# Performance work log

Measured on AMD Instinct MI355X. Metric: run time of the kernel, lower is better.

## Reference

```python
import jax, jax.numpy as jnp
import numpy as np

N = 20000      # nodes
E = 256000     # edges
H = 8          # heads
DIN = 256      # in_dim_struct / in_dim_semantic
DH = 32        # num_hidden per head (H*DH == DIN for GT residual)
PRED = 32      # pred_dim (relation embedding dim)
REL = 16       # rel_num
NEG = 0.2      # negative_slope for GAT attention
ALPHA = 0.5    # args.fusion
NUM_LAYERS = 2


def seg_softmax(e, seg, n):
    # softmax over edges grouped by destination node; e: [E, ...], seg: [E]
    m = jax.ops.segment_max(e, seg, num_segments=n)
    ex = jnp.exp(e - m[seg])
    s = jax.ops.segment_sum(ex, seg, num_segments=n)
    return ex / (s[seg] + 1e-9)


def setup_inputs() -> dict:
    key = jax.random.key(0)
    ks = jax.random.split(key, 24)
    f32 = jnp.float32
    def rn(k, shape, scale=0.05):
        return jax.random.normal(k, shape, dtype=f32) * scale
    return {
        "feats_struct": jax.random.normal(ks[0], (N, DIN), f32),
        "feats_semantic": jax.random.normal(ks[1], (N, DIN), f32),
        "centrality": jax.random.uniform(ks[2], (N,), f32),
        # fused per-head scoring MLP (heads[0] small Sequentials batched over H)
        "Ws1": rn(ks[3], (H, DIN, DIN // 2)),
        "bs1": jnp.zeros((H, DIN // 2), f32),
        "Ws2": rn(ks[4], (H, DIN // 2)),
        "bs2": jnp.zeros((H,), f32),
        "rel_emb": rn(ks[5], (REL, PRED), 1.0),
        # SALayer params (2 layers, per-head scalar channels)
        "sa_w": rn(ks[6], (NUM_LAYERS, H), 1.0),
        "sa_al": rn(ks[7], (NUM_LAYERS, H), 1.0),
        "sa_ar": rn(ks[8], (NUM_LAYERS, H), 1.0),
        "sa_We": rn(ks[9], (NUM_LAYERS, PRED, H)),
        # GTLayer params
        "Wq": rn(ks[10], (DIN, H * DH)),
        "bq": jnp.zeros((H * DH,), f32),
        "Wk": rn(ks[11], (DIN, H * DH)),
        "bk": jnp.zeros((H * DH,), f32),
        "Wv": rn(ks[12], (DIN, H * DH)),
        "bv": jnp.zeros((H * DH,), f32),
        "We_gt": rn(ks[13], (PRED, H * DH)),
        "bn_gamma": jnp.ones((H * DH,), f32),
        "bn_beta": jnp.zeros((H * DH,), f32),
        "Wout": rn(ks[14], (H * DH, 1)),
        "bout": jnp.zeros((1,), f32),
        # centrality scale params
        "gamma": jnp.ones((1, H), f32),
        "beta": jnp.zeros((1, H), f32),
        "edge_types": jax.random.randint(ks[15], (E,), 0, REL),
        "edge_src": jax.random.randint(ks[16], (E,), 0, N),
        "edge_dst": jax.random.randint(ks[17], (E,), 0, N),
    }


def _forward(feats_struct, feats_semantic, centrality, Ws1, bs1, Ws2, bs2,
             rel_emb, sa_w, sa_al, sa_ar, sa_We, Wq, bq, Wk, bk, Wv, bv,
             We_gt, bn_gamma, bn_beta, Wout, bout, gamma, beta,
             edge_types, edge_src, edge_dst):
    n = feats_struct.shape[0]
    edge_feats = rel_emb[edge_types]                                   # [E, PRED]

    # ---- structural channel: fused per-head scoring MLPs ----
    h1 = jax.nn.relu(jnp.einsum('nd,hdk->nhk', feats_struct, Ws1) + bs1)  # [N,H,DIN/2]
    h = jnp.einsum('nhk,hk->nh', h1, Ws2) + bs2                           # [N,H]

    # ---- SALayer stack (GAT-style, per-head scalar features) ----
    for l in range(NUM_LAYERS):
        z = h * sa_w[l]                                                 # [N,H]
        e = jax.nn.leaky_relu(z[edge_src] * sa_al[l] + z[edge_dst] * sa_ar[l]
                              + edge_feats @ sa_We[l], NEG)             # [E,H]
        attn = seg_softmax(e, edge_dst, n)                              # [E,H]
        out = jax.ops.segment_sum(attn * z[edge_src], edge_dst, num_segments=n)
        h = jax.nn.elu(out + z)                                         # residual + activation
        if l != NUM_LAYERS - 1:
            h = jnp.mean(h, axis=-1, keepdims=True)
            h = jnp.tile(h, (1, H))
    logits_struct = h                                                   # [N,H]

    # ---- semantic channel: Graph Transformer layer (edge_mode='MUL') ----
    q = (feats_semantic @ Wq + bq).reshape(n, H, DH)
    k = (feats_semantic @ Wk + bk).reshape(n, H, DH)
    v = (feats_semantic @ Wv + bv).reshape(n, H, DH)
    ep = (edge_feats @ We_gt).reshape(-1, H, DH)                        # [E,H,DH]
    ke = k[edge_src] * ep                                               # MUL edge gating
    score = jnp.sum(q[edge_dst] * ke, axis=-1) / jnp.sqrt(jnp.float32(DH))  # [E,H]
    attn = seg_softmax(score, edge_dst, n)                              # [E,H]
    agg = jax.ops.segment_sum(attn[..., None] * v[edge_src], edge_dst,
                              num_segments=n).reshape(n, H * DH)
    agg = agg + feats_semantic                                          # residual (H*DH == DIN)
    mu = jnp.mean(agg, axis=0)
    var = jnp.var(agg, axis=0)
    agg = (agg - mu) / jnp.sqrt(var + 1e-5) * bn_gamma + bn_beta        # batch norm
    h_sem = jax.nn.relu(agg)
    logits_semantic = h_sem @ Wout + bout                               # [N,1]

    # ---- fusion + centrality gamma/beta scaling ----
    logits = ALPHA * logits_struct + (1.0 - ALPHA) * logits_semantic    # [N,H]
    scaled = (centrality[:, None] * gamma + beta) * logits              # [N,H]
    return jax.nn.leaky_relu(jnp.mean(scaled, axis=-1, keepdims=True), 0.01)


def reference(feats_struct, feats_semantic, centrality, Ws1, bs1, Ws2, bs2,
              rel_emb, sa_w, sa_al, sa_ar, sa_We, Wq, bq, Wk, bk, Wv, bv,
              We_gt, bn_gamma, bn_beta, Wout, bout, gamma, beta,
              edge_types, edge_src, edge_dst):
    return _forward(feats_struct, feats_semantic, centrality, Ws1, bs1, Ws2, bs2,
                    rel_emb, sa_w, sa_al, sa_ar, sa_We, Wq, bq, Wk, bk, Wv, bv,
                    We_gt, bn_gamma, bn_beta, Wout, bout, gamma, beta,
                    edge_types, edge_src, edge_dst)
```

## Files before the change

kernel.cpp:

```cpp
#include <hip/hip_runtime.h>
#include <hip/hip_bf16.h>
#include <math.h>

#define N_NODES 20000
#define N_EDGES 256000

typedef __attribute__((ext_vector_type(8))) __bf16 bf16x8;
typedef __attribute__((ext_vector_type(8))) unsigned short u16x8;
typedef __attribute__((ext_vector_type(4))) float f32x4;

static __device__ __forceinline__ unsigned short f2bf(float f) {
  unsigned u = __float_as_uint(f);
  unsigned r = (u + 0x7fffu + ((u >> 16) & 1u)) >> 16;
  return (unsigned short)r;
}


__global__ void k_tables(const float* __restrict__ rel_emb,
                         const float* __restrict__ sa_We,
                         const float* __restrict__ We_gt,
                         float* __restrict__ saTab, float* __restrict__ epTab) {
  int t = threadIdx.x;
  {
    int l = t >> 7, r = (t >> 3) & 15, h = t & 7;
    float acc = 0.f;
    for (int p = 0; p < 32; ++p)
      acc += rel_emb[r * 32 + p] * sa_We[l * 256 + p * 8 + h];
    saTab[t] = acc;
  }
  for (int r = 0; r < 16; ++r) {
    float acc = 0.f;
    for (int p = 0; p < 32; ++p)
      acc += rel_emb[r * 32 + p] * We_gt[p * 256 + t];
    epTab[r * 256 + t] = acc;
  }
}

__global__ void k_hist(const int* __restrict__ e_dst, int* __restrict__ deg) {
  int e = blockIdx.x * 256 + threadIdx.x;
  if (e < N_EDGES) atomicAdd(&deg[e_dst[e]], 1);
}

__global__ void k_scan(const int* __restrict__ deg, int* __restrict__ rowPtr,
                       int* __restrict__ cursor) {
  const int CH = (N_NODES + 255) / 256;
  int t = threadIdx.x;
  int b0 = t * CH, b1 = min(b0 + CH, N_NODES);
  int s = 0;
  for (int i = b0; i < b1; ++i) s += deg[i];
  __shared__ int part[256];
  part[t] = s;
  __syncthreads();
  for (int off = 1; off < 256; off <<= 1) {
    int add = (t >= off) ? part[t - off] : 0;
    __syncthreads();
    part[t] += add;
    __syncthreads();
  }
  int run = (t == 0) ? 0 : part[t - 1];
  for (int i = b0; i < b1; ++i) {
    rowPtr[i] = run;
    cursor[i] = run;
    run += deg[i];
  }
  if (t == 0) rowPtr[N_NODES] = part[255];
}

__global__ void k_fill(const int* __restrict__ e_dst, const int* __restrict__ e_src,
                       const int* __restrict__ e_type, int* __restrict__ cursor,
                       int* __restrict__ csrSrc, int* __restrict__ csrType) {
  int e = blockIdx.x * 256 + threadIdx.x;
  if (e >= N_EDGES) return;
  int d = e_dst[e];
  int pos = atomicAdd(&cursor[d], 1);
  csrSrc[pos] = e_src[e];
  csrType[pos] = e_type[e];
}


__global__ void k_convX(const float* __restrict__ Xs, const float* __restrict__ Xm,
                        ushort* __restrict__ Xsb, ushort* __restrict__ Xmb) {
  size_t i = ((size_t)blockIdx.x * 256 + threadIdx.x) * 4;
  float4 a = *(const float4*)(Xs + i);
  ushort4 ua = {f2bf(a.x), f2bf(a.y), f2bf(a.z), f2bf(a.w)};
  *(ushort4*)(Xsb + i) = ua;
  float4 b = *(const float4*)(Xm + i);
  ushort4 ub = {f2bf(b.x), f2bf(b.y), f2bf(b.z), f2bf(b.w)};
  *(ushort4*)(Xmb + i) = ub;
}

__global__ void k_tws1(const float* __restrict__ Ws1, ushort* __restrict__ Ws1t) {
  int h = blockIdx.x >> 7, kcol = blockIdx.x & 127, d = threadIdx.x;
  Ws1t[((size_t)h * 128 + kcol) * 256 + d] = f2bf(Ws1[((size_t)h * 256 + d) * 128 + kcol]);
}

__global__ void k_twqkv(const float* __restrict__ Wq, const float* __restrict__ Wk,
                        const float* __restrict__ Wv, ushort* __restrict__ Wt) {
  int m = blockIdx.x >> 8, n = blockIdx.x & 255, d = threadIdx.x;
  const float* W = (m == 0) ? Wq : (m == 1) ? Wk : Wv;
  Wt[((size_t)m * 256 + n) * 256 + d] = f2bf(W[(size_t)d * 256 + n]);
}


__global__ __launch_bounds__(256) void k_mlp_mfma(
    const ushort* __restrict__ Xb, const ushort* __restrict__ Ws1t,
    const float* __restrict__ bs1, const float* __restrict__ Ws2,
    const float* __restrict__ bs2, float* __restrict__ h0) {
  __shared__ ushort Ab[64][136];
  __shared__ ushort Bb[128][136];
  int tid = threadIdx.x;
  int h = blockIdx.y;
  int base = blockIdx.x * 64;
  int wv = tid >> 6, lane = tid & 63;
  int l15 = lane & 15, lhi = lane >> 4;
  f32x4 acc[8];
  #pragma unroll
  for (int nt = 0; nt < 8; ++nt) acc[nt] = (f32x4){0.f, 0.f, 0.f, 0.f};

  for (int kc = 0; kc < 2; ++kc) {
    {
      int r = tid >> 2, c4 = (tid & 3) * 4;
      int gr = base + r;
      const ushort* src = Xb + (size_t)gr * 256 + kc * 128;
      #pragma unroll
      for (int s = 0; s < 4; ++s) {
        u16x8 val = {0, 0, 0, 0, 0, 0, 0, 0};
        if (gr < N_NODES) val = *(const u16x8*)(src + (c4 + s) * 8);
        *(u16x8*)&Ab[r][(c4 + s) * 8] = val;
      }
    }
    {
      int r = tid >> 1, cb = (tid & 1) * 8;
      const ushort* src = Ws1t + ((size_t)h * 128 + r) * 256 + kc * 128;
      #pragma unroll
      for (int s = 0; s < 8; ++s)
        *(u16x8*)&Bb[r][(cb + s) * 8] = *(const u16x8*)(src + (cb + s) * 8);
    }
    __syncthreads();
    #pragma unroll
    for (int kk = 0; kk < 4; ++kk) {
      bf16x8 a = *(const bf16x8*)&Ab[wv * 16 + l15][kk * 32 + lhi * 8];
      #pragma unroll
      for (int nt = 0; nt < 8; ++nt) {
        bf16x8 b = *(const bf16x8*)&Bb[nt * 16 + l15][kk * 32 + lhi * 8];
        acc[nt] = __builtin_amdgcn_mfma_f32_16x16x32_bf16(a, b, acc[nt], 0, 0, 0);
      }
    }
    __syncthreads();
  }
  float part[4] = {0.f, 0.f, 0.f, 0.f};
  #pragma unroll
  for (int nt = 0; nt < 8; ++nt) {
    int c = h * 128 + nt * 16 + l15;
    float b1 = bs1[c], w2 = Ws2[c];
    #pragma unroll
    for (int j = 0; j < 4; ++j)
      part[j] += fmaxf(acc[nt][j] + b1, 0.f) * w2;
  }
  #pragma unroll
  for (int j = 0; j < 4; ++j) {
    #pragma unroll
    for (int o = 1; o < 16; o <<= 1) part[j] += __shfl_xor(part[j], o);
  }
  if (l15 == 0) {
    float b2 = bs2[h];
    #pragma unroll
    for (int j = 0; j < 4; ++j) {
      int row = base + wv * 16 + lhi * 4 + j;
      if (row < N_NODES) h0[(size_t)row * 8 + h] = part[j] + b2;
    }
  }
}


__global__ __launch_bounds__(256) void k_qkv_mfma(
    const ushort* __restrict__ Xb, const ushort* __restrict__ Wt,
    const float* __restrict__ bq, const float* __restrict__ bk,
    const float* __restrict__ bv, float* __restrict__ q,
    float* __restrict__ k, float* __restrict__ v) {
  __shared__ ushort Ab[64][136];
  __shared__ ushort Bb[128][136];
  int tid = threadIdx.x;
  int m = blockIdx.y >> 1, half = blockIdx.y & 1;
  int base = blockIdx.x * 64;
  int wv = tid >> 6, lane = tid & 63;
  int l15 = lane & 15, lhi = lane >> 4;
  f32x4 acc[8];
  #pragma unroll
  for (int nt = 0; nt < 8; ++nt) acc[nt] = (f32x4){0.f, 0.f, 0.f, 0.f};

  for (int kc = 0; kc < 2; ++kc) {
    {
      int r = tid >> 2, c4 = (tid & 3) * 4;
      int gr = base + r;
      const ushort* src = Xb + (size_t)gr * 256 + kc * 128;
      #pragma unroll
      for (int s = 0; s < 4; ++s) {
        u16x8 val = {0, 0, 0, 0, 0, 0, 0, 0};
        if (gr < N_NODES) val = *(const u16x8*)(src + (c4 + s) * 8);
        *(u16x8*)&Ab[r][(c4 + s) * 8] = val;
      }
    }
    {
      int r = tid >> 1, cb = (tid & 1) * 8;
      const ushort* src = Wt + (((size_t)m * 256 + half * 128 + r) * 256) + kc * 128;
      #pragma unroll
      for (int s = 0; s < 8; ++s)
        *(u16x8*)&Bb[r][(cb + s) * 8] = *(const u16x8*)(src + (cb + s) * 8);
    }
    __syncthreads();
    #pragma unroll
    for (int kk = 0; kk < 4; ++kk) {
      bf16x8 a = *(const bf16x8*)&Ab[wv * 16 + l15][kk * 32 + lhi * 8];
      #pragma unroll
      for (int nt = 0; nt < 8; ++nt) {
        bf16x8 b = *(const bf16x8*)&Bb[nt * 16 + l15][kk * 32 + lhi * 8];
        acc[nt] = __builtin_amdgcn_mfma_f32_16x16x32_bf16(a, b, acc[nt], 0, 0, 0);
      }
    }
    __syncthreads();
  }
  float* out = (m == 0) ? q : (m == 1) ? k : v;
  const float* bias = (m == 0) ? bq : (m == 1) ? bk : bv;
  #pragma unroll
  for (int nt = 0; nt < 8; ++nt) {
    int c = half * 128 + nt * 16 + l15;
    float bc = bias[c];
    #pragma unroll
    for (int j = 0; j < 4; ++j) {
      int row = base + wv * 16 + lhi * 4 + j;
      if (row < N_NODES) out[(size_t)row * 256 + c] = acc[nt][j] + bc;
    }
  }
}


__global__ __launch_bounds__(256) void k_sa(const float* __restrict__ h_in,
                                            float* __restrict__ h_out,
                                            const int* __restrict__ rowPtr,
                                            const int* __restrict__ csrSrc,
                                            const int* __restrict__ csrType,
                                            const float* __restrict__ sa_w,
                                            const float* __restrict__ sa_al,
                                            const float* __restrict__ sa_ar,
                                            const float* __restrict__ saTab, int layer) {
  int t = blockIdx.x * 256 + threadIdx.x;
  int node = t >> 3, h = t & 7;
  float wgt = sa_w[layer * 8 + h];
  float al = sa_al[layer * 8 + h];
  float ar = sa_ar[layer * 8 + h];
  const float* tab = saTab + layer * 128;
  float zd = h_in[node * 8 + h] * wgt;
  int s0 = rowPtr[node], s1 = rowPtr[node + 1];
  float m = -INFINITY, lsum = 0.f, acc = 0.f;
  for (int i = s0; i < s1; ++i) {
    int s = csrSrc[i], ty = csrType[i];
    float zs = h_in[s * 8 + h] * wgt;
    float e = zs * al + zd * ar + tab[ty * 8 + h];
    e = (e >= 0.f) ? e : 0.2f * e;
    float nm = fmaxf(m, e);
    float scl = expf(m - nm);
    float p = expf(e - nm);
    acc = acc * scl + p * zs;
    lsum = lsum * scl + p;
    m = nm;
  }
  float o = acc / (lsum + 1e-9f);
  float r = o + zd;
  r = (r > 0.f) ? r : expm1f(r);
  if (layer == 0) {
    r += __shfl_xor(r, 1);
    r += __shfl_xor(r, 2);
    r += __shfl_xor(r, 4);
    r *= 0.125f;
  }
  h_out[node * 8 + h] = r;
}


__global__ __launch_bounds__(256) void k_gt(const float* __restrict__ q,
                                            const float* __restrict__ k,
                                            const float* __restrict__ v,
                                            const float* __restrict__ epTab,
                                            const float* __restrict__ feats_sem,
                                            const int* __restrict__ rowPtr,
                                            const int* __restrict__ csrSrc,
                                            const int* __restrict__ csrType,
                                            float* __restrict__ agg) {
  int node = blockIdx.x * 4 + (threadIdx.x >> 6);
  int lane = threadIdx.x & 63;
  int c0 = lane * 4;
  const float SC = 0.17677669529663687f;
  float4 qv = *(const float4*)(q + (size_t)node * 256 + c0);
  qv.x *= SC; qv.y *= SC; qv.z *= SC; qv.w *= SC;
  float4 acc = {0.f, 0.f, 0.f, 0.f};
  float m = -INFINITY, lsum = 0.f;
  int s0 = rowPtr[node], s1 = rowPtr[node + 1];
  for (int i = s0; i < s1; ++i) {
    int s = csrSrc[i], ty = csrType[i];
    float4 kv = *(const float4*)(k + (size_t)s * 256 + c0);
    float4 ep = *(const float4*)(epTab + ty * 256 + c0);
    float part = qv.x * kv.x * ep.x + qv.y * kv.y * ep.y +
                 qv.z * kv.z * ep.z + qv.w * kv.w * ep.w;
    part += __shfl_xor(part, 1);
    part += __shfl_xor(part, 2);
    part += __shfl_xor(part, 4);
    float nm = fmaxf(m, part);
    float scl = expf(m - nm);
    float p = expf(part - nm);
    float4 vv = *(const float4*)(v + (size_t)s * 256 + c0);
    acc.x = acc.x * scl + p * vv.x;
    acc.y = acc.y * scl + p * vv.y;
    acc.z = acc.z * scl + p * vv.z;
    acc.w = acc.w * scl + p * vv.w;
    lsum = lsum * scl + p;
    m = nm;
  }
  float inv = 1.f / (lsum + 1e-9f);
  float4 fs = *(const float4*)(feats_sem + (size_t)node * 256 + c0);
  float4 r;
  r.x = acc.x * inv + fs.x;
  r.y = acc.y * inv + fs.y;
  r.z = acc.z * inv + fs.z;
  r.w = acc.w * inv + fs.w;
  *(float4*)(agg + (size_t)node * 256 + c0) = r;
}

__global__ void k_bnstats(const float* __restrict__ agg, double* __restrict__ colsum,
                          double* __restrict__ colssq) {
  int t = threadIdx.x;
  int r0 = blockIdx.x * 79;
  int r1 = min(r0 + 79, N_NODES);
  double s = 0.0, qq = 0.0;
  for (int r = r0; r < r1; ++r) {
    float x = agg[(size_t)r * 256 + t];
    s += (double)x;
    qq += (double)x * (double)x;
  }
  atomicAdd(&colsum[t], s);
  atomicAdd(&colssq[t], qq);
}

__global__ void k_bnfinal(const double* __restrict__ colsum, const double* __restrict__ colssq,
                          float* __restrict__ muArr, float* __restrict__ invArr) {
  int t = threadIdx.x;
  double mu = colsum[t] / (double)N_NODES;
  double var = colssq[t] / (double)N_NODES - mu * mu;
  muArr[t] = (float)mu;
  invArr[t] = (float)(1.0 / sqrt(var + 1e-5));
}

__global__ __launch_bounds__(256) void k_final(const float* __restrict__ agg,
                                               const float* __restrict__ muArr,
                                               const float* __restrict__ invArr,
                                               const float* __restrict__ bn_gamma,
                                               const float* __restrict__ bn_beta,
                                               const float* __restrict__ Wout,
                                               const float* __restrict__ bout,
                                               const float* __restrict__ hB,
                                               const float* __restrict__ cent,
                                               const float* __restrict__ gamma,
                                               const float* __restrict__ beta,
                                               float* __restrict__ out) {
  int node = blockIdx.x * 4 + (threadIdx.x >> 6);
  int lane = threadIdx.x & 63;
  int c0 = lane * 4;
  float4 x = *(const float4*)(agg + (size_t)node * 256 + c0);
  float4 mu = *(const float4*)(muArr + c0);
  float4 iv = *(const float4*)(invArr + c0);
  float4 g = *(const float4*)(bn_gamma + c0);
  float4 b = *(const float4*)(bn_beta + c0);
  float4 w = *(const float4*)(Wout + c0);
  float p = fmaxf((x.x - mu.x) * iv.x * g.x + b.x, 0.f) * w.x +
            fmaxf((x.y - mu.y) * iv.y * g.y + b.y, 0.f) * w.y +
            fmaxf((x.z - mu.z) * iv.z * g.z + b.z, 0.f) * w.z +
            fmaxf((x.w - mu.w) * iv.w * g.w + b.w, 0.f) * w.w;
  #pragma unroll
  for (int o = 1; o < 64; o <<= 1) p += __shfl_xor(p, o);
  float ls = p + bout[0];
  int h = lane & 7;
  float logit = 0.5f * hB[(size_t)node * 8 + h] + 0.5f * ls;
  float sc = (cent[node] * gamma[h] + beta[h]) * logit;
  sc += __shfl_xor(sc, 1);
  sc += __shfl_xor(sc, 2);
  sc += __shfl_xor(sc, 4);
  float mn = sc * 0.125f;
  mn = (mn >= 0.f) ? mn : 0.01f * mn;
  if (lane == 0) out[node] = mn;
}


extern "C" void kernel_launch(void* const* d_in, const int* in_sizes, int n_in,
                              void* d_out, int out_size, void* d_ws, size_t ws_size,
                              hipStream_t stream) {
  (void)in_sizes; (void)n_in; (void)out_size; (void)ws_size;
  const float* feats_struct = (const float*)d_in[0];
  const float* feats_sem    = (const float*)d_in[1];
  const float* cent         = (const float*)d_in[2];
  const float* Ws1          = (const float*)d_in[3];
  const float* bs1          = (const float*)d_in[4];
  const float* Ws2          = (const float*)d_in[5];
  const float* bs2          = (const float*)d_in[6];
  const float* rel_emb      = (const float*)d_in[7];
  const float* sa_w         = (const float*)d_in[8];
  const float* sa_al        = (const float*)d_in[9];
  const float* sa_ar        = (const float*)d_in[10];
  const float* sa_We        = (const float*)d_in[11];
  const float* Wq           = (const float*)d_in[12];
  const float* bq           = (const float*)d_in[13];
  const float* Wk           = (const float*)d_in[14];
  const float* bk           = (const float*)d_in[15];
  const float* Wv           = (const float*)d_in[16];
  const float* bv           = (const float*)d_in[17];
  const float* We_gt        = (const float*)d_in[18];
  const float* bn_gamma     = (const float*)d_in[19];
  const float* bn_beta      = (const float*)d_in[20];
  const float* Wout         = (const float*)d_in[21];
  const float* bout         = (const float*)d_in[22];
  const float* gamma        = (const float*)d_in[23];
  const float* beta         = (const float*)d_in[24];
  const int* e_type         = (const int*)d_in[25];
  const int* e_src          = (const int*)d_in[26];
  const int* e_dst          = (const int*)d_in[27];
  float* out = (float*)d_out;

  char* wsb = (char*)d_ws;
  size_t off = 0;
  auto alloc = [&](size_t bytes) -> char* {
    char* p = wsb + off;
    off = (off + bytes + 255) & ~(size_t)255;
    return p;
  };
  float* saTab   = (float*)alloc(2 * 16 * 8 * 4);
  float* epTab   = (float*)alloc(16 * 256 * 4);
  int* deg       = (int*)alloc((size_t)N_NODES * 4);
  int* rowPtr    = (int*)alloc((size_t)(N_NODES + 1) * 4);
  int* cursor    = (int*)alloc((size_t)N_NODES * 4);
  int* csrSrc    = (int*)alloc((size_t)N_EDGES * 4);
  int* csrType   = (int*)alloc((size_t)N_EDGES * 4);
  float* h0      = (float*)alloc((size_t)N_NODES * 8 * 4);
  float* hA      = (float*)alloc((size_t)N_NODES * 8 * 4);
  float* hB      = (float*)alloc((size_t)N_NODES * 8 * 4);
  float* qb      = (float*)alloc((size_t)N_NODES * 256 * 4);
  float* kb      = (float*)alloc((size_t)N_NODES * 256 * 4);
  float* vb      = (float*)alloc((size_t)N_NODES * 256 * 4);
  float* agg     = (float*)alloc((size_t)N_NODES * 256 * 4);
  double* colsum = (double*)alloc(256 * 8);
  double* colssq = (double*)alloc(256 * 8);
  float* muArr   = (float*)alloc(256 * 4);
  float* invArr  = (float*)alloc(256 * 4);
  ushort* Xsb    = (ushort*)alloc((size_t)N_NODES * 256 * 2);
  ushort* Xmb    = (ushort*)alloc((size_t)N_NODES * 256 * 2);
  ushort* Ws1t   = (ushort*)alloc((size_t)8 * 128 * 256 * 2);
  ushort* Wqkvt  = (ushort*)alloc((size_t)3 * 256 * 256 * 2);

  hipMemsetAsync(deg, 0, (size_t)N_NODES * 4, stream);
  hipMemsetAsync(colsum, 0, 256 * 8, stream);
  hipMemsetAsync(colssq, 0, 256 * 8, stream);

  k_tables<<<1, 256, 0, stream>>>(rel_emb, sa_We, We_gt, saTab, epTab);
  k_hist<<<(N_EDGES + 255) / 256, 256, 0, stream>>>(e_dst, deg);
  k_scan<<<1, 256, 0, stream>>>(deg, rowPtr, cursor);
  k_fill<<<(N_EDGES + 255) / 256, 256, 0, stream>>>(e_dst, e_src, e_type, cursor, csrSrc, csrType);

  k_convX<<<N_NODES * 256 / (256 * 4), 256, 0, stream>>>(feats_struct, feats_sem, Xsb, Xmb);
  k_tws1<<<8 * 128, 256, 0, stream>>>(Ws1, Ws1t);
  k_twqkv<<<3 * 256, 256, 0, stream>>>(Wq, Wk, Wv, Wqkvt);

  const int MT = (N_NODES + 63) / 64;
  dim3 gMlp(MT, 8);
  k_mlp_mfma<<<gMlp, 256, 0, stream>>>(Xsb, Ws1t, bs1, Ws2, bs2, h0);
  k_sa<<<N_NODES * 8 / 256, 256, 0, stream>>>(h0, hA, rowPtr, csrSrc, csrType,
                                              sa_w, sa_al, sa_ar, saTab, 0);
  k_sa<<<N_NODES * 8 / 256, 256, 0, stream>>>(hA, hB, rowPtr, csrSrc, csrType,
                                              sa_w, sa_al, sa_ar, saTab, 1);

  dim3 gQkv(MT, 6);
  k_qkv_mfma<<<gQkv, 256, 0, stream>>>(Xmb, Wqkvt, bq, bk, bv, qb, kb, vb);
  k_gt<<<N_NODES / 4, 256, 0, stream>>>(qb, kb, vb, epTab, feats_sem,
                                        rowPtr, csrSrc, csrType, agg);
  k_bnstats<<<256, 256, 0, stream>>>(agg, colsum, colssq);
  k_bnfinal<<<1, 256, 0, stream>>>(colsum, colssq, muArr, invArr);
  k_final<<<N_NODES / 4, 256, 0, stream>>>(agg, muArr, invArr, bn_gamma, bn_beta,
                                           Wout, bout, hB, cent, gamma, beta, out);
}
```

Before: 440.6 us.

## Store K/V in bf16, unroll GT edge loop by two, parallelize SA over edges

The QKV GEMM now writes K and V as bf16, halving the bytes gathered per edge in the graph-transformer attention. The GT loop handles two edges per iteration, so more independent loads are in flight. The SA kernel now gives each node a full wavefront with 8 edge slots per head and merges the partial online-softmax states with shuffles, raising parallelism for the high-degree gather. The cost is reduced K/V precision, plus extra exp and shuffle work in the SA merge.

```diff
diff --git a/kernel.cpp b/kernel.cpp
--- a/kernel.cpp
+++ b/kernel.cpp
@@ -13,6 +13,9 @@
   unsigned u = __float_as_uint(f);
   unsigned r = (u + 0x7fffu + ((u >> 16) & 1u)) >> 16;
   return (unsigned short)r;
+}
+static __device__ __forceinline__ float b2f(unsigned short u) {
+  return __uint_as_float((unsigned)u << 16);
 }
 
 
@@ -177,7 +180,7 @@
     const ushort* __restrict__ Xb, const ushort* __restrict__ Wt,
     const float* __restrict__ bq, const float* __restrict__ bk,
     const float* __restrict__ bv, float* __restrict__ q,
-    float* __restrict__ k, float* __restrict__ v) {
+    ushort* __restrict__ kb, ushort* __restrict__ vb) {
   __shared__ ushort Ab[64][136];
   __shared__ ushort Bb[128][136];
   int tid = threadIdx.x;
@@ -220,7 +223,6 @@
     }
     __syncthreads();
   }
-  float* out = (m == 0) ? q : (m == 1) ? k : v;
   const float* bias = (m == 0) ? bq : (m == 1) ? bk : bv;
   #pragma unroll
   for (int nt = 0; nt < 8; ++nt) {
@@ -229,7 +231,12 @@
     #pragma unroll
     for (int j = 0; j < 4; ++j) {
       int row = base + wv * 16 + lhi * 4 + j;
-      if (row < N_NODES) out[(size_t)row * 256 + c] = acc[nt][j] + bc;
+      if (row < N_NODES) {
+        float val = acc[nt][j] + bc;
+        if (m == 0) q[(size_t)row * 256 + c] = val;
+        else if (m == 1) kb[(size_t)row * 256 + c] = f2bf(val);
+        else vb[(size_t)row * 256 + c] = f2bf(val);
+      }
     }
   }
 }
@@ -244,18 +251,19 @@
                                             const float* __restrict__ sa_al,
                                             const float* __restrict__ sa_ar,
                                             const float* __restrict__ saTab, int layer) {
-  int t = blockIdx.x * 256 + threadIdx.x;
-  int node = t >> 3, h = t & 7;
+  int node = blockIdx.x * 4 + (threadIdx.x >> 6);
+  int lane = threadIdx.x & 63;
+  int h = lane & 7, eslot = lane >> 3;
   float wgt = sa_w[layer * 8 + h];
   float al = sa_al[layer * 8 + h];
   float ar = sa_ar[layer * 8 + h];
   const float* tab = saTab + layer * 128;
-  float zd = h_in[node * 8 + h] * wgt;
+  float zd = h_in[(size_t)node * 8 + h] * wgt;
   int s0 = rowPtr[node], s1 = rowPtr[node + 1];
-  float m = -INFINITY, lsum = 0.f, acc = 0.f;
-  for (int i = s0; i < s1; ++i) {
+  float m = -1e30f, lsum = 0.f, acc = 0.f;
+  for (int i = s0 + eslot; i < s1; i += 8) {
     int s = csrSrc[i], ty = csrType[i];
-    float zs = h_in[s * 8 + h] * wgt;
+    float zs = h_in[(size_t)s * 8 + h] * wgt;
     float e = zs * al + zd * ar + tab[ty * 8 + h];
     e = (e >= 0.f) ? e : 0.2f * e;
     float nm = fmaxf(m, e);
@@ -265,6 +273,18 @@
     lsum = lsum * scl + p;
     m = nm;
   }
+  #pragma unroll
+  for (int off = 8; off < 64; off <<= 1) {
+    float om = __shfl_xor(m, off);
+    float ol = __shfl_xor(lsum, off);
+    float oa = __shfl_xor(acc, off);
+    float nm = fmaxf(m, om);
+    float sl = expf(m - nm);
+    float so = expf(om - nm);
+    acc = acc * sl + oa * so;
+    lsum = lsum * sl + ol * so;
+    m = nm;
+  }
   float o = acc / (lsum + 1e-9f);
   float r = o + zd;
   r = (r > 0.f) ? r : expm1f(r);
@@ -274,13 +294,13 @@
     r += __shfl_xor(r, 4);
     r *= 0.125f;
   }
-  h_out[node * 8 + h] = r;
+  if (eslot == 0) h_out[(size_t)node * 8 + h] = r;
 }
 
 
 __global__ __launch_bounds__(256) void k_gt(const float* __restrict__ q,
-                                            const float* __restrict__ k,
-                                            const float* __restrict__ v,
+                                            const ushort* __restrict__ kb,
+                                            const ushort* __restrict__ vb,
                                             const float* __restrict__ epTab,
                                             const float* __restrict__ feats_sem,
                                             const int* __restrict__ rowPtr,
@@ -294,25 +314,53 @@
   float4 qv = *(const float4*)(q + (size_t)node * 256 + c0);
   qv.x *= SC; qv.y *= SC; qv.z *= SC; qv.w *= SC;
   float4 acc = {0.f, 0.f, 0.f, 0.f};
-  float m = -INFINITY, lsum = 0.f;
+  float m = -1e30f, lsum = 0.f;
   int s0 = rowPtr[node], s1 = rowPtr[node + 1];
-  for (int i = s0; i < s1; ++i) {
+  int i = s0;
+  for (; i + 1 < s1; i += 2) {
+    int sA = csrSrc[i], tyA = csrType[i];
+    int sB = csrSrc[i + 1], tyB = csrType[i + 1];
+    ushort4 kA = *(const ushort4*)(kb + (size_t)sA * 256 + c0);
+    ushort4 kB4 = *(const ushort4*)(kb + (size_t)sB * 256 + c0);
+    float4 epA = *(const float4*)(epTab + tyA * 256 + c0);
+    float4 epB = *(const float4*)(epTab + tyB * 256 + c0);
+    ushort4 vA = *(const ushort4*)(vb + (size_t)sA * 256 + c0);
+    ushort4 vB = *(const ushort4*)(vb + (size_t)sB * 256 + c0);
+    float pA = qv.x * b2f(kA.x) * epA.x + qv.y * b2f(kA.y) * epA.y +
+               qv.z * b2f(kA.z) * epA.z + qv.w * b2f(kA.w) * epA.w;
+    float pB = qv.x * b2f(kB4.x) * epB.x + qv.y * b2f(kB4.y) * epB.y +
+               qv.z * b2f(kB4.z) * epB.z + qv.w * b2f(kB4.w) * epB.w;
+    pA += __shfl_xor(pA, 1); pB += __shfl_xor(pB, 1);
+    pA += __shfl_xor(pA, 2); pB += __shfl_xor(pB, 2);
+    pA += __shfl_xor(pA, 4); pB += __shfl_xor(pB, 4);
+    float nm = fmaxf(m, fmaxf(pA, pB));
+    float scl = expf(m - nm);
+    float eA = expf(pA - nm);
+    float eB = expf(pB - nm);
+    acc.x = acc.x * scl + eA * b2f(vA.x) + eB * b2f(vB.x);
+    acc.y = acc.y * scl + eA * b2f(vA.y) + eB * b2f(vB.y);
+    acc.z = acc.z * scl + eA * b2f(vA.z) + eB * b2f(vB.z);
+    acc.w = acc.w * scl + eA * b2f(vA.w) + eB * b2f(vB.w);
+    lsum = lsum * scl + eA + eB;
+    m = nm;
+  }
+  if (i < s1) {
     int s = csrSrc[i], ty = csrType[i];
-    float4 kv = *(const float4*)(k + (size_t)s * 256 + c0);
+    ushort4 kv = *(const ushort4*)(kb + (size_t)s * 256 + c0);
     float4 ep = *(const float4*)(epTab + ty * 256 + c0);
-    float part = qv.x * kv.x * ep.x + qv.y * kv.y * ep.y +
-                 qv.z * kv.z * ep.z + qv.w * kv.w * ep.w;
+    ushort4 vv = *(const ushort4*)(vb + (size_t)s * 256 + c0);
+    float part = qv.x * b2f(kv.x) * ep.x + qv.y * b2f(kv.y) * ep.y +
+                 qv.z * b2f(kv.z) * ep.z + qv.w * b2f(kv.w) * ep.w;
     part += __shfl_xor(part, 1);
     part += __shfl_xor(part, 2);
     part += __shfl_xor(part, 4);
     float nm = fmaxf(m, part);
     float scl = expf(m - nm);
     float p = expf(part - nm);
-    float4 vv = *(const float4*)(v + (size_t)s * 256 + c0);
-    acc.x = acc.x * scl + p * vv.x;
-    acc.y = acc.y * scl + p * vv.y;
-    acc.z = acc.z * scl + p * vv.z;
-    acc.w = acc.w * scl + p * vv.w;
+    acc.x = acc.x * scl + p * b2f(vv.x);
+    acc.y = acc.y * scl + p * b2f(vv.y);
+    acc.z = acc.z * scl + p * b2f(vv.z);
+    acc.w = acc.w * scl + p * b2f(vv.w);
     lsum = lsum * scl + p;
     m = nm;
   }
@@ -442,8 +490,8 @@
   float* hA      = (float*)alloc((size_t)N_NODES * 8 * 4);
   float* hB      = (float*)alloc((size_t)N_NODES * 8 * 4);
   float* qb      = (float*)alloc((size_t)N_NODES * 256 * 4);
-  float* kb      = (float*)alloc((size_t)N_NODES * 256 * 4);
-  float* vb      = (float*)alloc((size_t)N_NODES * 256 * 4);
+  ushort* kbB    = (ushort*)alloc((size_t)N_NODES * 256 * 2);
+  ushort* vbB    = (ushort*)alloc((size_t)N_NODES * 256 * 2);
   float* agg     = (float*)alloc((size_t)N_NODES * 256 * 4);
   double* colsum = (double*)alloc(256 * 8);
   double* colssq = (double*)alloc(256 * 8);
@@ -470,14 +518,14 @@
   const int MT = (N_NODES + 63) / 64;
   dim3 gMlp(MT, 8);
   k_mlp_mfma<<<gMlp, 256, 0, stream>>>(Xsb, Ws1t, bs1, Ws2, bs2, h0);
-  k_sa<<<N_NODES * 8 / 256, 256, 0, stream>>>(h0, hA, rowPtr, csrSrc, csrType,
+  k_sa<<<(N_NODES + 3) / 4, 256, 0, stream>>>(h0, hA, rowPtr, csrSrc, csrType,
                                               sa_w, sa_al, sa_ar, saTab, 0);
-  k_sa<<<N_NODES * 8 / 256, 256, 0, stream>>>(hA, hB, rowPtr, csrSrc, csrType,
+  k_sa<<<(N_NODES + 3) / 4, 256, 0, stream>>>(hA, hB, rowPtr, csrSrc, csrType,
                                               sa_w, sa_al, sa_ar, saTab, 1);
 
   dim3 gQkv(MT, 6);
-  k_qkv_mfma<<<gQkv, 256, 0, stream>>>(Xmb, Wqkvt, bq, bk, bv, qb, kb, vb);
-  k_gt<<<N_NODES / 4, 256, 0, stream>>>(qb, kb, vb, epTab, feats_sem,
+  k_qkv_mfma<<<gQkv, 256, 0, stream>>>(Xmb, Wqkvt, bq, bk, bv, qb, kbB, vbB);
+  k_gt<<<N_NODES / 4, 256, 0, stream>>>(qb, kbB, vbB, epTab, feats_sem,
                                         rowPtr, csrSrc, csrType, agg);
   k_bnstats<<<256, 256, 0, stream>>>(agg, colsum, colssq);
   k_bnfinal<<<1, 256, 0, stream>>>(colsum, colssq, muArr, invArr);
```

Result: faster. 402.0 us (-8.8%).
